# Optimization experiments

Hardware: AMD Instinct MI355X
Metric: run time of the kernel (lower is better)

Reference implementation:

```python
import jax, jax.numpy as jnp
import numpy as np

T, B, NIN, NH = 2048, 16, 1024, 1024
G = 4 * NH  # gate size


def setup_inputs() -> dict:
    key = jax.random.key(0)
    k1, k2, k3, k4 = jax.random.split(key, 4)
    stdv = 1.0 / np.sqrt(NH)
    X = jax.random.normal(k1, (T, B, NIN), dtype=jnp.float32)
    i = jnp.ones((T, B), dtype=jnp.float32)  # all-valid mask
    h0 = jnp.zeros((B, NH), dtype=jnp.float32)
    c0 = jnp.zeros((B, NH), dtype=jnp.float32)
    W_in = jax.random.uniform(k2, (NIN, G), minval=-stdv, maxval=stdv, dtype=jnp.float32)
    W_re = jax.random.uniform(k3, (NH, G), minval=-stdv, maxval=stdv, dtype=jnp.float32)
    b = jax.random.uniform(k4, (G,), minval=-2 * stdv, maxval=2 * stdv, dtype=jnp.float32)
    return {"X": X, "i": i, "h0": h0, "c0": c0, "W_in": W_in, "W_re": W_re, "b": b}


def reference(X, i, h0, c0, W_in, W_re, b):
    # intern = X @ W_in + b, precomputed for all timesteps (big GEMM)
    H = W_re.shape[0]
    intern = jnp.einsum('tbi,ig->tbg', X, W_in) + b  # [T,B,4H]

    def step(carry, inp):
        h, c = carry
        z, m = inp                       # z: [B,4H], m: [B]
        z = z + h @ W_re                 # recurrent contribution
        cell_in = jnp.tanh(z[:, :H])
        in_gate = jax.nn.sigmoid(z[:, H:2 * H])
        fgt_gate = jax.nn.sigmoid(z[:, 2 * H:3 * H])
        out_gate = jax.nn.sigmoid(z[:, 3 * H:])
        c_new = fgt_gate * c + in_gate * cell_in
        y_new = out_gate * jnp.tanh(c_new)
        m = m[:, None]
        c = m * c_new + (1.0 - m) * c    # masked frames keep old cell
        y = m * y_new                    # masked frames output zero
        return (y, c), (y, c)

    (_, d), (Y, C) = jax.lax.scan(step, (h0, c0), (intern, i))
    # Y: [T,B,H] outputs; C: [T,B,H] per-step cell states; d: [B,H] final cell
    return Y, C, d
```

## Files before the change

kernel.cpp:

```cpp
#include <hip/hip_runtime.h>
#include <cstdint>
#include <cstddef>

#define T_STEPS 2048
#define BATCH   16
#define NIN_D   1024
#define NH_D    1024
#define G_D     4096
#define MROWS   32768
#define NWG     64
#define WGT     512
#define PWORDS  8192

typedef short short8 __attribute__((ext_vector_type(8)));
typedef float f32x4  __attribute__((ext_vector_type(4)));
typedef unsigned u32x4 __attribute__((ext_vector_type(4)));

__device__ __forceinline__ unsigned short f2bf(float f) {
  unsigned u = __builtin_bit_cast(unsigned, f);
  u += 0x7FFFu + ((u >> 16) & 1u);
  return (unsigned short)(u >> 16);
}
__device__ __forceinline__ float bf2f(unsigned short h) {
  unsigned u = ((unsigned)h) << 16;
  return __builtin_bit_cast(float, u);
}
__device__ __forceinline__ float sigmoidf_(float x) { return 1.0f / (1.0f + __expf(-x)); }
__device__ __forceinline__ float tanhf_(float x)    { return 2.0f / (1.0f + __expf(-2.0f * x)) - 1.0f; }

__global__ void cast_f32_bf16(const float* __restrict__ in, unsigned short* __restrict__ out, int n4) {
  int idx = blockIdx.x * blockDim.x + threadIdx.x;
  if (idx < n4) {
    float4 v = ((const float4*)in)[idx];
    ushort4 o;
    o.x = f2bf(v.x); o.y = f2bf(v.y); o.z = f2bf(v.z); o.w = f2bf(v.w);
    ((ushort4*)out)[idx] = o;
  }
}

__global__ void transpose_cast(const float* __restrict__ in, unsigned short* __restrict__ out) {
  __shared__ float tile[32][33];
  const int gx = blockIdx.x * 32;
  const int gy = blockIdx.y * 32;
  const int tx = threadIdx.x, ty = threadIdx.y;
  #pragma unroll
  for (int p = 0; p < 4; ++p)
    tile[ty + p * 8][tx] = in[(size_t)(gy + ty + p * 8) * G_D + gx + tx];
  __syncthreads();
  #pragma unroll
  for (int p = 0; p < 4; ++p)
    out[(size_t)(gx + ty + p * 8) * NIN_D + gy + tx] = f2bf(tile[tx][ty + p * 8]);
}

__global__ void init_hseq(const float* __restrict__ h0, u32x4* __restrict__ hs) {
  const int nq = (T_STEPS * PWORDS) / 4;
  for (int q = blockIdx.x * blockDim.x + threadIdx.x; q < nq; q += gridDim.x * blockDim.x) {
    u32x4 v;
    if (q < PWORDS / 4) {
      #pragma unroll
      for (int u = 0; u < 4; ++u) {
        unsigned lo = f2bf(h0[8 * q + 2 * u]);
        unsigned hi = f2bf(h0[8 * q + 2 * u + 1]);
        lo = (lo == 0xFFFFu) ? 0xFFFEu : lo;
        hi = (hi == 0xFFFFu) ? 0xFFFEu : hi;
        v[u] = lo | (hi << 16);
      }
    } else {
      v = (u32x4){0xFFFFFFFFu, 0xFFFFFFFFu, 0xFFFFFFFFu, 0xFFFFFFFFu};
    }
    hs[q] = v;
  }
}

__global__ __launch_bounds__(256) void gemm_intern(
    const unsigned short* __restrict__ A,
    const unsigned short* __restrict__ Bt,
    const float* __restrict__ bias,
    unsigned short* __restrict__ Out) {
  __shared__ unsigned short As[128 * 72];
  __shared__ unsigned short Bs[128 * 72];
  const int tid  = threadIdx.x;
  const int lane = tid & 63;
  const int w    = tid >> 6;
  const int r16  = lane & 15;
  const int kgrp = lane >> 4;
  const int wrow = (w >> 1) * 64;
  const int wcol = (w & 1) * 64;
  const int bx = blockIdx.x;
  const int by = blockIdx.y;

  const unsigned short* Ag = A  + (size_t)by * 128 * NIN_D;
  const unsigned short* Bg = Bt + (size_t)bx * 128 * NIN_D;
  const int trow = tid >> 3;
  const int tcol = (tid & 7) * 8;

  f32x4 acc[4][4];
  #pragma unroll
  for (int m = 0; m < 4; ++m)
    #pragma unroll
    for (int n = 0; n < 4; ++n)
      acc[m][n] = (f32x4){0.f, 0.f, 0.f, 0.f};

  for (int kt = 0; kt < 16; ++kt) {
    const int kb = kt * 64;
    __syncthreads();
    #pragma unroll
    for (int p = 0; p < 4; ++p) {
      const int r = trow + p * 32;
      *(uint4*)(&As[r * 72 + tcol]) = *(const uint4*)(Ag + (size_t)r * NIN_D + kb + tcol);
      *(uint4*)(&Bs[r * 72 + tcol]) = *(const uint4*)(Bg + (size_t)r * NIN_D + kb + tcol);
    }
    __syncthreads();
    #pragma unroll
    for (int kk = 0; kk < 2; ++kk) {
      const int ko = kk * 32 + kgrp * 8;
      short8 af[4], bq[4];
      #pragma unroll
      for (int m = 0; m < 4; ++m)
        af[m] = *(const short8*)(&As[(wrow + m * 16 + r16) * 72 + ko]);
      #pragma unroll
      for (int n = 0; n < 4; ++n)
        bq[n] = *(const short8*)(&Bs[(wcol + n * 16 + r16) * 72 + ko]);
      #pragma unroll
      for (int m = 0; m < 4; ++m)
        #pragma unroll
        for (int n = 0; n < 4; ++n)
          acc[m][n] = __builtin_amdgcn_mfma_f32_16x16x32_bf16(af[m], bq[n], acc[m][n], 0, 0, 0);
    }
  }
  #pragma unroll
  for (int n = 0; n < 4; ++n) {
    const int col = bx * 128 + wcol + n * 16 + r16;
    const float bv = bias[col];
    #pragma unroll
    for (int m = 0; m < 4; ++m) {
      const int row0 = by * 128 + wrow + m * 16 + kgrp * 4;
      #pragma unroll
      for (int i = 0; i < 4; ++i)
        Out[(size_t)(row0 + i) * G_D + col] = f2bf(acc[m][n][i] + bv);
    }
  }
}

__device__ __forceinline__ bool fresh4_(u32x4 v) {
  bool ok = true;
  #pragma unroll
  for (int u = 0; u < 4; ++u)
    ok = ok && ((v[u] & 0xFFFFu) != 0xFFFFu) && ((v[u] >> 16) != 0xFFFFu);
  return ok;
}
__device__ __forceinline__ void poll_stage(const unsigned* __restrict__ buf, int tid,
                                           unsigned short* __restrict__ h_s) {
  u32x4 a0, a1, a2, a3;
  const unsigned* p0 = buf + (0 * WGT + tid) * 4;
  const unsigned* p1 = buf + (1 * WGT + tid) * 4;
  const unsigned* p2 = buf + (2 * WGT + tid) * 4;
  const unsigned* p3 = buf + (3 * WGT + tid) * 4;
  bool done = false, first = true;
  do {
    if (!done) {
      if (!first) __builtin_amdgcn_s_sleep(1);
      first = false;
      asm volatile(
          "global_load_dwordx4 %0, %4, off sc0 sc1\n\t"
          "global_load_dwordx4 %1, %5, off sc0 sc1\n\t"
          "global_load_dwordx4 %2, %6, off sc0 sc1\n\t"
          "global_load_dwordx4 %3, %7, off sc0 sc1\n\t"
          "s_waitcnt vmcnt(0)"
          : "=v"(a0), "=v"(a1), "=v"(a2), "=v"(a3)
          : "v"(p0), "v"(p1), "v"(p2), "v"(p3)
          : "memory");
      done = fresh4_(a0) && fresh4_(a1) && fresh4_(a2) && fresh4_(a3);
    }
  } while (!__all((int)done));
#define STG(i, A) { const int Qi = (i) * WGT + tid; \
    *(u32x4*)((char*)h_s + (Qi >> 7) * 2064 + (Qi & 127) * 16) = A; }
  STG(0, a0) STG(1, a1) STG(2, a2) STG(3, a3)
#undef STG
}

__global__ __launch_bounds__(WGT, 2) void lstm_scan(
    const unsigned short* __restrict__ intern,
    const unsigned short* __restrict__ WreT,
    const float* __restrict__ msk,
    const float* __restrict__ c0,
    unsigned* __restrict__ hseq,
    float* __restrict__ Y, float* __restrict__ C, float* __restrict__ D) {
  const int wg = blockIdx.x;
  const int tid = threadIdx.x;
  const int wv = tid >> 6, lane = tid & 63;
  const int r16 = lane & 15, kgrp = lane >> 4;
  const int ks = wv >> 1, gp = wv & 1;
  const int j0 = wg * 16;

  __shared__ __attribute__((aligned(16))) unsigned short h_s[16 * 1032];
  __shared__ __attribute__((aligned(16))) float z_s[4][4][16][20];

  short8 wfrag[2][8];
  #pragma unroll
  for (int g2 = 0; g2 < 2; ++g2) {
    const unsigned short* wp =
        WreT + (size_t)((2 * gp + g2) * NH_D + j0 + r16) * NH_D + ks * 256 + kgrp * 8;
    #pragma unroll
    for (int kc = 0; kc < 8; ++kc)
      wfrag[g2][kc] = *(const short8*)(wp + kc * 32);
  }

  const int b = tid >> 4, jj = tid & 15;
  const bool gt = tid < 256;
  float creg = 0.f, mreg = 0.f;
  unsigned short ipr[4] = {0, 0, 0, 0};
  if (gt) {
    creg = c0[b * NH_D + j0 + jj];
    mreg = msk[b];
    #pragma unroll
    for (int g = 0; g < 4; ++g)
      ipr[g] = intern[(size_t)b * G_D + g * NH_D + j0 + jj];
  }

  poll_stage(hseq, tid, h_s);
  __syncthreads();

  for (int t = 0; t < T_STEPS; ++t) {
    f32x4 acc0 = (f32x4){0.f, 0.f, 0.f, 0.f};
    f32x4 acc1 = (f32x4){0.f, 0.f, 0.f, 0.f};
    const int hbase = r16 * 1032 + ks * 256 + kgrp * 8;
    #pragma unroll
    for (int kc = 0; kc < 8; ++kc) {
      short8 a = *(const short8*)(&h_s[hbase + kc * 32]);
      acc0 = __builtin_amdgcn_mfma_f32_16x16x32_bf16(a, wfrag[0][kc], acc0, 0, 0, 0);
      acc1 = __builtin_amdgcn_mfma_f32_16x16x32_bf16(a, wfrag[1][kc], acc1, 0, 0, 0);
    }
    *(f32x4*)&z_s[ks][2 * gp + 0][r16][kgrp * 4] = acc0;
    *(f32x4*)&z_s[ks][2 * gp + 1][r16][kgrp * 4] = acc1;
    __syncthreads();

    if (gt) {
      float zq[4];
      #pragma unroll
      for (int g = 0; g < 4; ++g)
        zq[g] = ((z_s[0][g][jj][b] + z_s[1][g][jj][b]) +
                 (z_s[2][g][jj][b] + z_s[3][g][jj][b])) + bf2f(ipr[g]);
      const float cell = tanhf_(zq[0]);
      const float ig = sigmoidf_(zq[1]);
      const float fg = sigmoidf_(zq[2]);
      const float og = sigmoidf_(zq[3]);
      const float cn = fg * creg + ig * cell;
      const float yn = og * tanhf_(cn);
      const float cnew = mreg * cn + (1.0f - mreg) * creg;
      const float ynew = mreg * yn;
      creg = cnew;

      if (t < T_STEPS - 1) {
        const unsigned short yb = f2bf(ynew);
        const unsigned prt = (unsigned)(unsigned short)__shfl_xor((int)(unsigned)yb, 1);
        if ((tid & 1) == 0) {
          unsigned* dst = hseq + (size_t)(t + 1) * PWORDS;
          __hip_atomic_store(&dst[b * 512 + ((j0 + jj) >> 1)],
                             ((unsigned)yb) | (prt << 16),
                             __ATOMIC_RELAXED, __HIP_MEMORY_SCOPE_AGENT);
        }
      }
      const size_t ob = ((size_t)t * BATCH + b) * NH_D + j0 + jj;
      __builtin_nontemporal_store(ynew, &Y[ob]);
      __builtin_nontemporal_store(cnew, &C[ob]);
      if (t < T_STEPS - 1) {
        const unsigned short* ipn = intern + ((size_t)(t + 1) * BATCH + b) * G_D;
        #pragma unroll
        for (int g = 0; g < 4; ++g)
          ipr[g] = ipn[g * NH_D + j0 + jj];
        mreg = msk[(t + 1) * BATCH + b];
      }
    }

    if (t < T_STEPS - 1)
      poll_stage(hseq + (size_t)(t + 1) * PWORDS, tid, h_s);
    __syncthreads();
  }
  if (gt) D[b * NH_D + j0 + jj] = creg;
}

extern "C" void kernel_launch(void* const* d_in, const int* in_sizes, int n_in,
                              void* d_out, int out_size, void* d_ws, size_t ws_size,
                              hipStream_t stream) {
  const float* X     = (const float*)d_in[0];
  const float* imask = (const float*)d_in[1];
  const float* h0    = (const float*)d_in[2];
  const float* c0    = (const float*)d_in[3];
  const float* Win   = (const float*)d_in[4];
  const float* Wre   = (const float*)d_in[5];
  const float* bias  = (const float*)d_in[6];
  float* out = (float*)d_out;

  char* ws = (char*)d_ws;
  unsigned short* Xbf    = (unsigned short*)(ws);
  unsigned short* WinT   = (unsigned short*)(ws + 67108864);
  unsigned short* WreT   = (unsigned short*)(ws + 75497472);
  unsigned short* intern = (unsigned short*)(ws + 83886080);
  unsigned*       hseq   = (unsigned*)(ws);

  float* Y = out;
  float* C = out + (size_t)T_STEPS * BATCH * NH_D;
  float* D = out + (size_t)2 * T_STEPS * BATCH * NH_D;

  {
    int n4 = (MROWS * NIN_D) / 4;
    cast_f32_bf16<<<dim3((n4 + 255) / 256), dim3(256), 0, stream>>>(X, Xbf, n4);
  }
  transpose_cast<<<dim3(G_D / 32, NIN_D / 32), dim3(32, 8), 0, stream>>>(Win, WinT);
  transpose_cast<<<dim3(G_D / 32, NH_D / 32),  dim3(32, 8), 0, stream>>>(Wre, WreT);

  gemm_intern<<<dim3(G_D / 128, MROWS / 128), dim3(256), 0, stream>>>(Xbf, WinT, bias, intern);

  init_hseq<<<dim3(1024), dim3(256), 0, stream>>>(h0, (u32x4*)hseq);

  lstm_scan<<<dim3(NWG), dim3(WGT), 0, stream>>>(intern, WreT, imask, c0, hseq, Y, C, D);
}
```

Before: 6.213 ms.

## Load recurrent h fragments directly from global into registers, drop LDS staging barrier

Each wave now polls the published hidden-state buffer straight into the MFMA A-operand registers in fragment layout, instead of cooperatively staging it through an LDS tile. This removes the LDS writes and reads plus the second __syncthreads per timestep. The gate-partial scratch is double-buffered by step parity so the remaining single barrier is sufficient. The next step's poll is issued at the end of the iteration and only waited on at the top. Each wave now loads the full h row slice it needs, which changes the global access pattern and adds redundant reads across waves that share the same k-slice.

```diff
diff --git a/kernel.cpp b/kernel.cpp
--- a/kernel.cpp
+++ b/kernel.cpp
@@ -142,41 +142,25 @@
   }
 }
 
+#define POLL8(P) asm volatile( \
+    "global_load_dwordx4 %0, %8, off sc0 sc1\n\t" \
+    "global_load_dwordx4 %1, %8, off offset:64 sc0 sc1\n\t" \
+    "global_load_dwordx4 %2, %8, off offset:128 sc0 sc1\n\t" \
+    "global_load_dwordx4 %3, %8, off offset:192 sc0 sc1\n\t" \
+    "global_load_dwordx4 %4, %8, off offset:256 sc0 sc1\n\t" \
+    "global_load_dwordx4 %5, %8, off offset:320 sc0 sc1\n\t" \
+    "global_load_dwordx4 %6, %8, off offset:384 sc0 sc1\n\t" \
+    "global_load_dwordx4 %7, %8, off offset:448 sc0 sc1" \
+    : "=v"(q0), "=v"(q1), "=v"(q2), "=v"(q3), \
+      "=v"(q4), "=v"(q5), "=v"(q6), "=v"(q7) \
+    : "v"(P) : "memory")
+
 __device__ __forceinline__ bool fresh4_(u32x4 v) {
   bool ok = true;
   #pragma unroll
   for (int u = 0; u < 4; ++u)
     ok = ok && ((v[u] & 0xFFFFu) != 0xFFFFu) && ((v[u] >> 16) != 0xFFFFu);
   return ok;
-}
-__device__ __forceinline__ void poll_stage(const unsigned* __restrict__ buf, int tid,
-                                           unsigned short* __restrict__ h_s) {
-  u32x4 a0, a1, a2, a3;
-  const unsigned* p0 = buf + (0 * WGT + tid) * 4;
-  const unsigned* p1 = buf + (1 * WGT + tid) * 4;
-  const unsigned* p2 = buf + (2 * WGT + tid) * 4;
-  const unsigned* p3 = buf + (3 * WGT + tid) * 4;
-  bool done = false, first = true;
-  do {
-    if (!done) {
-      if (!first) __builtin_amdgcn_s_sleep(1);
-      first = false;
-      asm volatile(
-          "global_load_dwordx4 %0, %4, off sc0 sc1\n\t"
-          "global_load_dwordx4 %1, %5, off sc0 sc1\n\t"
-          "global_load_dwordx4 %2, %6, off sc0 sc1\n\t"
-          "global_load_dwordx4 %3, %7, off sc0 sc1\n\t"
-          "s_waitcnt vmcnt(0)"
-          : "=v"(a0), "=v"(a1), "=v"(a2), "=v"(a3)
-          : "v"(p0), "v"(p1), "v"(p2), "v"(p3)
-          : "memory");
-      done = fresh4_(a0) && fresh4_(a1) && fresh4_(a2) && fresh4_(a3);
-    }
-  } while (!__all((int)done));
-#define STG(i, A) { const int Qi = (i) * WGT + tid; \
-    *(u32x4*)((char*)h_s + (Qi >> 7) * 2064 + (Qi & 127) * 16) = A; }
-  STG(0, a0) STG(1, a1) STG(2, a2) STG(3, a3)
-#undef STG
 }
 
 __global__ __launch_bounds__(WGT, 2) void lstm_scan(
@@ -193,8 +177,7 @@
   const int ks = wv >> 1, gp = wv & 1;
   const int j0 = wg * 16;
 
-  __shared__ __attribute__((aligned(16))) unsigned short h_s[16 * 1032];
-  __shared__ __attribute__((aligned(16))) float z_s[4][4][16][20];
+  __shared__ __attribute__((aligned(16))) float z_s[2][4][4][16][20];
 
   short8 wfrag[2][8];
   #pragma unroll
@@ -218,29 +201,58 @@
       ipr[g] = intern[(size_t)b * G_D + g * NH_D + j0 + jj];
   }
 
-  poll_stage(hseq, tid, h_s);
-  __syncthreads();
+  const int poffw = r16 * 512 + ks * 128 + kgrp * 4;
+
+  u32x4 q0, q1, q2, q3, q4, q5, q6, q7;
+  POLL8(hseq + poffw);
 
   for (int t = 0; t < T_STEPS; ++t) {
+    const int par = t & 1;
+    const unsigned* pb = hseq + (size_t)t * PWORDS + poffw;
+
+    for (;;) {
+      asm volatile("s_waitcnt vmcnt(0)" ::: "memory");
+      __builtin_amdgcn_sched_barrier(0);
+      bool ok = fresh4_(q0) && fresh4_(q1) && fresh4_(q2) && fresh4_(q3)
+             && fresh4_(q4) && fresh4_(q5) && fresh4_(q6) && fresh4_(q7);
+      if (__all((int)ok)) break;
+      POLL8(pb);
+    }
+
+    short8 a0 = __builtin_bit_cast(short8, q0), a1 = __builtin_bit_cast(short8, q1);
+    short8 a2 = __builtin_bit_cast(short8, q2), a3 = __builtin_bit_cast(short8, q3);
+    short8 a4 = __builtin_bit_cast(short8, q4), a5 = __builtin_bit_cast(short8, q5);
+    short8 a6 = __builtin_bit_cast(short8, q6), a7 = __builtin_bit_cast(short8, q7);
+
     f32x4 acc0 = (f32x4){0.f, 0.f, 0.f, 0.f};
     f32x4 acc1 = (f32x4){0.f, 0.f, 0.f, 0.f};
-    const int hbase = r16 * 1032 + ks * 256 + kgrp * 8;
-    #pragma unroll
-    for (int kc = 0; kc < 8; ++kc) {
-      short8 a = *(const short8*)(&h_s[hbase + kc * 32]);
-      acc0 = __builtin_amdgcn_mfma_f32_16x16x32_bf16(a, wfrag[0][kc], acc0, 0, 0, 0);
-      acc1 = __builtin_amdgcn_mfma_f32_16x16x32_bf16(a, wfrag[1][kc], acc1, 0, 0, 0);
-    }
-    *(f32x4*)&z_s[ks][2 * gp + 0][r16][kgrp * 4] = acc0;
-    *(f32x4*)&z_s[ks][2 * gp + 1][r16][kgrp * 4] = acc1;
+    acc0 = __builtin_amdgcn_mfma_f32_16x16x32_bf16(a0, wfrag[0][0], acc0, 0, 0, 0);
+    acc1 = __builtin_amdgcn_mfma_f32_16x16x32_bf16(a0, wfrag[1][0], acc1, 0, 0, 0);
+    acc0 = __builtin_amdgcn_mfma_f32_16x16x32_bf16(a1, wfrag[0][1], acc0, 0, 0, 0);
+    acc1 = __builtin_amdgcn_mfma_f32_16x16x32_bf16(a1, wfrag[1][1], acc1, 0, 0, 0);
+    acc0 = __builtin_amdgcn_mfma_f32_16x16x32_bf16(a2, wfrag[0][2], acc0, 0, 0, 0);
+    acc1 = __builtin_amdgcn_mfma_f32_16x16x32_bf16(a2, wfrag[1][2], acc1, 0, 0, 0);
+    acc0 = __builtin_amdgcn_mfma_f32_16x16x32_bf16(a3, wfrag[0][3], acc0, 0, 0, 0);
+    acc1 = __builtin_amdgcn_mfma_f32_16x16x32_bf16(a3, wfrag[1][3], acc1, 0, 0, 0);
+    acc0 = __builtin_amdgcn_mfma_f32_16x16x32_bf16(a4, wfrag[0][4], acc0, 0, 0, 0);
+    acc1 = __builtin_amdgcn_mfma_f32_16x16x32_bf16(a4, wfrag[1][4], acc1, 0, 0, 0);
+    acc0 = __builtin_amdgcn_mfma_f32_16x16x32_bf16(a5, wfrag[0][5], acc0, 0, 0, 0);
+    acc1 = __builtin_amdgcn_mfma_f32_16x16x32_bf16(a5, wfrag[1][5], acc1, 0, 0, 0);
+    acc0 = __builtin_amdgcn_mfma_f32_16x16x32_bf16(a6, wfrag[0][6], acc0, 0, 0, 0);
+    acc1 = __builtin_amdgcn_mfma_f32_16x16x32_bf16(a6, wfrag[1][6], acc1, 0, 0, 0);
+    acc0 = __builtin_amdgcn_mfma_f32_16x16x32_bf16(a7, wfrag[0][7], acc0, 0, 0, 0);
+    acc1 = __builtin_amdgcn_mfma_f32_16x16x32_bf16(a7, wfrag[1][7], acc1, 0, 0, 0);
+
+    *(f32x4*)&z_s[par][ks][2 * gp + 0][r16][kgrp * 4] = acc0;
+    *(f32x4*)&z_s[par][ks][2 * gp + 1][r16][kgrp * 4] = acc1;
     __syncthreads();
 
     if (gt) {
       float zq[4];
       #pragma unroll
       for (int g = 0; g < 4; ++g)
-        zq[g] = ((z_s[0][g][jj][b] + z_s[1][g][jj][b]) +
-                 (z_s[2][g][jj][b] + z_s[3][g][jj][b])) + bf2f(ipr[g]);
+        zq[g] = ((z_s[par][0][g][jj][b] + z_s[par][1][g][jj][b]) +
+                 (z_s[par][2][g][jj][b] + z_s[par][3][g][jj][b])) + bf2f(ipr[g]);
       const float cell = tanhf_(zq[0]);
       const float ig = sigmoidf_(zq[1]);
       const float fg = sigmoidf_(zq[2]);
@@ -274,8 +286,7 @@
     }
 
     if (t < T_STEPS - 1)
-      poll_stage(hseq + (size_t)(t + 1) * PWORDS, tid, h_s);
-    __syncthreads();
+      POLL8(hseq + (size_t)(t + 1) * PWORDS + poffw);
   }
   if (gt) D[b * NH_D + j0 + jj] = creg;
 }
```

Result: slower. 10.04 ms (+61.5%).

## Split recurrent K across all 8 waves with per-wave h polling, drop barrier

Applied to the files above, without the earlier changes.

Changes the LSTM scan so each of the 8 waves owns a 128-wide K slice for all four gates. Each wave polls only its own slice of the published h vector, stages it in a private LDS tile, and runs the MFMAs without waiting on the other waves. The hseq publish layout is permuted so every wave's slice is contiguous, letting one base address with offsets serve the poll. The next step's poll loads are issued before the waitcnt, which overlaps them with the rest of the loop and removes one __syncthreads per step. The cost is an 8-way partial-sum reduction in LDS instead of 4-way, and a larger z_s buffer.

```diff
diff --git a/kernel.cpp b/kernel.cpp
--- a/kernel.cpp
+++ b/kernel.cpp
@@ -54,13 +54,16 @@
 
 __global__ void init_hseq(const float* __restrict__ h0, u32x4* __restrict__ hs) {
   const int nq = (T_STEPS * PWORDS) / 4;
-  for (int q = blockIdx.x * blockDim.x + threadIdx.x; q < nq; q += gridDim.x * blockDim.x) {
+  for (int q4 = blockIdx.x * blockDim.x + threadIdx.x; q4 < nq; q4 += gridDim.x * blockDim.x) {
     u32x4 v;
-    if (q < PWORDS / 4) {
+    if (q4 < PWORDS / 4) {
+      const int w0 = q4 * 4;
+      const int wg = w0 >> 7, b = (w0 >> 3) & 15, q0 = w0 & 7;
+      const float* hb = h0 + b * NH_D + wg * 16 + q0 * 2;
       #pragma unroll
       for (int u = 0; u < 4; ++u) {
-        unsigned lo = f2bf(h0[8 * q + 2 * u]);
-        unsigned hi = f2bf(h0[8 * q + 2 * u + 1]);
+        unsigned lo = f2bf(hb[2 * u]);
+        unsigned hi = f2bf(hb[2 * u + 1]);
         lo = (lo == 0xFFFFu) ? 0xFFFEu : lo;
         hi = (hi == 0xFFFFu) ? 0xFFFEu : hi;
         v[u] = lo | (hi << 16);
@@ -68,7 +71,7 @@
     } else {
       v = (u32x4){0xFFFFFFFFu, 0xFFFFFFFFu, 0xFFFFFFFFu, 0xFFFFFFFFu};
     }
-    hs[q] = v;
+    hs[q4] = v;
   }
 }
 
@@ -142,41 +145,20 @@
   }
 }
 
+#define POLL4(P) asm volatile( \
+    "global_load_dwordx4 %0, %4, off sc0 sc1\n\t" \
+    "global_load_dwordx4 %1, %4, off offset:1024 sc0 sc1\n\t" \
+    "global_load_dwordx4 %2, %4, off offset:2048 sc0 sc1\n\t" \
+    "global_load_dwordx4 %3, %4, off offset:3072 sc0 sc1" \
+    : "=v"(a0), "=v"(a1), "=v"(a2), "=v"(a3) \
+    : "v"(P) : "memory")
+
 __device__ __forceinline__ bool fresh4_(u32x4 v) {
   bool ok = true;
   #pragma unroll
   for (int u = 0; u < 4; ++u)
     ok = ok && ((v[u] & 0xFFFFu) != 0xFFFFu) && ((v[u] >> 16) != 0xFFFFu);
   return ok;
-}
-__device__ __forceinline__ void poll_stage(const unsigned* __restrict__ buf, int tid,
-                                           unsigned short* __restrict__ h_s) {
-  u32x4 a0, a1, a2, a3;
-  const unsigned* p0 = buf + (0 * WGT + tid) * 4;
-  const unsigned* p1 = buf + (1 * WGT + tid) * 4;
-  const unsigned* p2 = buf + (2 * WGT + tid) * 4;
-  const unsigned* p3 = buf + (3 * WGT + tid) * 4;
-  bool done = false, first = true;
-  do {
-    if (!done) {
-      if (!first) __builtin_amdgcn_s_sleep(1);
-      first = false;
-      asm volatile(
-          "global_load_dwordx4 %0, %4, off sc0 sc1\n\t"
-          "global_load_dwordx4 %1, %5, off sc0 sc1\n\t"
-          "global_load_dwordx4 %2, %6, off sc0 sc1\n\t"
-          "global_load_dwordx4 %3, %7, off sc0 sc1\n\t"
-          "s_waitcnt vmcnt(0)"
-          : "=v"(a0), "=v"(a1), "=v"(a2), "=v"(a3)
-          : "v"(p0), "v"(p1), "v"(p2), "v"(p3)
-          : "memory");
-      done = fresh4_(a0) && fresh4_(a1) && fresh4_(a2) && fresh4_(a3);
-    }
-  } while (!__all((int)done));
-#define STG(i, A) { const int Qi = (i) * WGT + tid; \
-    *(u32x4*)((char*)h_s + (Qi >> 7) * 2064 + (Qi & 127) * 16) = A; }
-  STG(0, a0) STG(1, a1) STG(2, a2) STG(3, a3)
-#undef STG
 }
 
 __global__ __launch_bounds__(WGT, 2) void lstm_scan(
@@ -190,20 +172,19 @@
   const int tid = threadIdx.x;
   const int wv = tid >> 6, lane = tid & 63;
   const int r16 = lane & 15, kgrp = lane >> 4;
-  const int ks = wv >> 1, gp = wv & 1;
   const int j0 = wg * 16;
 
-  __shared__ __attribute__((aligned(16))) unsigned short h_s[16 * 1032];
-  __shared__ __attribute__((aligned(16))) float z_s[4][4][16][20];
-
-  short8 wfrag[2][8];
-  #pragma unroll
-  for (int g2 = 0; g2 < 2; ++g2) {
+  __shared__ __attribute__((aligned(16))) unsigned short h_w[8][16][132];
+  __shared__ __attribute__((aligned(16))) float z_s[8][4][16][20];
+
+  short8 wfrag[4][4];
+  #pragma unroll
+  for (int g = 0; g < 4; ++g) {
     const unsigned short* wp =
-        WreT + (size_t)((2 * gp + g2) * NH_D + j0 + r16) * NH_D + ks * 256 + kgrp * 8;
-    #pragma unroll
-    for (int kc = 0; kc < 8; ++kc)
-      wfrag[g2][kc] = *(const short8*)(wp + kc * 32);
+        WreT + (size_t)(g * NH_D + j0 + r16) * NH_D + wv * 128 + kgrp * 8;
+    #pragma unroll
+    for (int kc = 0; kc < 4; ++kc)
+      wfrag[g][kc] = *(const short8*)(wp + kc * 32);
   }
 
   const int b = tid >> 4, jj = tid & 15;
@@ -218,29 +199,58 @@
       ipr[g] = intern[(size_t)b * G_D + g * NH_D + j0 + jj];
   }
 
-  poll_stage(hseq, tid, h_s);
-  __syncthreads();
+  const int pboff = wv * 4096 + lane * 16;
+  const int stg_b = (lane >> 1) & 15;
+  const int stg_j = ((lane >> 5) << 4) + ((lane & 1) << 3);
+  const int pubw = (wg << 7) | (b << 3) | (jj >> 1);
+
+  u32x4 a0, a1, a2, a3;
+  POLL4((const char*)hseq + pboff);
 
   for (int t = 0; t < T_STEPS; ++t) {
-    f32x4 acc0 = (f32x4){0.f, 0.f, 0.f, 0.f};
-    f32x4 acc1 = (f32x4){0.f, 0.f, 0.f, 0.f};
-    const int hbase = r16 * 1032 + ks * 256 + kgrp * 8;
-    #pragma unroll
-    for (int kc = 0; kc < 8; ++kc) {
-      short8 a = *(const short8*)(&h_s[hbase + kc * 32]);
-      acc0 = __builtin_amdgcn_mfma_f32_16x16x32_bf16(a, wfrag[0][kc], acc0, 0, 0, 0);
-      acc1 = __builtin_amdgcn_mfma_f32_16x16x32_bf16(a, wfrag[1][kc], acc1, 0, 0, 0);
-    }
-    *(f32x4*)&z_s[ks][2 * gp + 0][r16][kgrp * 4] = acc0;
-    *(f32x4*)&z_s[ks][2 * gp + 1][r16][kgrp * 4] = acc1;
+    const char* pl = (const char*)(hseq + (size_t)t * PWORDS) + pboff;
+
+    for (;;) {
+      asm volatile("s_waitcnt vmcnt(0)" ::: "memory");
+      __builtin_amdgcn_sched_barrier(0);
+      bool ok = fresh4_(a0) && fresh4_(a1) && fresh4_(a2) && fresh4_(a3);
+      if (__all((int)ok)) break;
+      __builtin_amdgcn_s_sleep(1);
+      POLL4(pl);
+    }
+
+    *(u32x4*)&h_w[wv][stg_b][stg_j]      = a0;
+    *(u32x4*)&h_w[wv][stg_b][stg_j + 32] = a1;
+    *(u32x4*)&h_w[wv][stg_b][stg_j + 64] = a2;
+    *(u32x4*)&h_w[wv][stg_b][stg_j + 96] = a3;
+
+    short8 af[4];
+    #pragma unroll
+    for (int kc = 0; kc < 4; ++kc)
+      af[kc] = *(const short8*)(&h_w[wv][r16][kc * 32 + kgrp * 8]);
+
+    f32x4 acc[4];
+    #pragma unroll
+    for (int g = 0; g < 4; ++g) acc[g] = (f32x4){0.f, 0.f, 0.f, 0.f};
+    #pragma unroll
+    for (int kc = 0; kc < 4; ++kc)
+      #pragma unroll
+      for (int g = 0; g < 4; ++g)
+        acc[g] = __builtin_amdgcn_mfma_f32_16x16x32_bf16(af[kc], wfrag[g][kc], acc[g], 0, 0, 0);
+
+    #pragma unroll
+    for (int g = 0; g < 4; ++g)
+      *(f32x4*)&z_s[wv][g][r16][kgrp * 4] = acc[g];
     __syncthreads();
 
     if (gt) {
       float zq[4];
       #pragma unroll
-      for (int g = 0; g < 4; ++g)
-        zq[g] = ((z_s[0][g][jj][b] + z_s[1][g][jj][b]) +
-                 (z_s[2][g][jj][b] + z_s[3][g][jj][b])) + bf2f(ipr[g]);
+      for (int g = 0; g < 4; ++g) {
+        float s0 = (z_s[0][g][jj][b] + z_s[1][g][jj][b]) + (z_s[2][g][jj][b] + z_s[3][g][jj][b]);
+        float s1 = (z_s[4][g][jj][b] + z_s[5][g][jj][b]) + (z_s[6][g][jj][b] + z_s[7][g][jj][b]);
+        zq[g] = s0 + s1 + bf2f(ipr[g]);
+      }
       const float cell = tanhf_(zq[0]);
       const float ig = sigmoidf_(zq[1]);
       const float fg = sigmoidf_(zq[2]);
@@ -256,8 +266,7 @@
         const unsigned prt = (unsigned)(unsigned short)__shfl_xor((int)(unsigned)yb, 1);
         if ((tid & 1) == 0) {
           unsigned* dst = hseq + (size_t)(t + 1) * PWORDS;
-          __hip_atomic_store(&dst[b * 512 + ((j0 + jj) >> 1)],
-                             ((unsigned)yb) | (prt << 16),
+          __hip_atomic_store(&dst[pubw], ((unsigned)yb) | (prt << 16),
                              __ATOMIC_RELAXED, __HIP_MEMORY_SCOPE_AGENT);
         }
       }
@@ -274,8 +283,7 @@
     }
 
     if (t < T_STEPS - 1)
-      poll_stage(hseq + (size_t)(t + 1) * PWORDS, tid, h_s);
-    __syncthreads();
+      POLL4((const char*)(hseq + (size_t)(t + 1) * PWORDS) + pboff);
   }
   if (gt) D[b * NH_D + j0 + jj] = creg;
 }
```

New measurement: 6.230 ms. About the same (+0.3%).
